# Kernel tuning notes

Hardware: AMD Instinct MI355X
Metric: run time of the kernel (lower is better)

## Reference

```python
import jax, jax.numpy as jnp
import numpy as np

ALPHA = 0.2  # leakyrelu negative slope

def setup_inputs() -> dict:
    key = jax.random.key(0)
    k1, k2, k3 = jax.random.split(key, 3)
    N, F_in, F_out = 8192, 512, 256
    input_x = jax.random.normal(k1, (N, F_in), dtype=jnp.float32)
    # xavier-ish scaling for params
    W = jax.random.normal(k2, (F_in, F_out), dtype=jnp.float32) * (1.414 * (2.0 / (F_in + F_out)) ** 0.5)
    a = jax.random.normal(k3, (2 * F_out, 1), dtype=jnp.float32) * (1.414 * (2.0 / (2 * F_out + 1)) ** 0.5)
    return {"input_x": input_x, "W": W, "a": a}

def reference(input_x, W, a):
    # h: [N, F_out]
    h = input_x @ W
    F_out = W.shape[1]
    # e_ij = leakyrelu([h_i || h_j] @ a) = leakyrelu(h_i @ a1 + h_j @ a2)
    s1 = h @ a[:F_out, 0]   # [N] contribution of row node i
    s2 = h @ a[F_out:, 0]   # [N] contribution of col node j
    e = jax.nn.leaky_relu(s1[:, None] + s2[None, :], negative_slope=ALPHA)  # [N, N]
    attention = jax.nn.softmax(e, axis=1)
    # dropout p=0.0 (eval) -> identity
    h_prime = attention @ h  # [N, F_out]
    return jax.nn.elu(h_prime)  # concat=True
```

## Files before the change

### kernel.cpp

```cpp
#include <hip/hip_runtime.h>
#include <hip/hip_bf16.h>

#define N_NODES 8192
#define F_IN    512
#define F_OUT   256
#define ALPHA   0.2f
#define CHUNK   32
#define NCHUNK  (N_NODES / CHUNK)
#define SEG     1024
#define BM      128
#define BN      64
#define BK      16

__global__ __launch_bounds__(512) void gemm_h(const float* __restrict__ A,
                                              const float* __restrict__ B,
                                              float* __restrict__ C) {
    __shared__ float As[BK][BM + 4];
    __shared__ float Bs[BK][BN + 4];
    const int t  = threadIdx.x;
    const int m0 = blockIdx.y * BM;
    const int n0 = blockIdx.x * BN;

    const int ar = t >> 2;
    const int ak = (t & 3) * 4;
    const int br = t >> 4;
    const int bc = (t & 15) * 4;

    const int ty = t >> 4;
    const int tx = t & 15;

    float4 aReg = *(const float4*)(A + (size_t)(m0 + ar) * F_IN + ak);
    float4 bReg = make_float4(0.f, 0.f, 0.f, 0.f);
    if (t < 256) bReg = *(const float4*)(B + (size_t)br * F_OUT + n0 + bc);

    float acc[4][4] = {};

    for (int k0 = 0; k0 < F_IN; k0 += BK) {
        __syncthreads();
        As[ak + 0][ar] = aReg.x;
        As[ak + 1][ar] = aReg.y;
        As[ak + 2][ar] = aReg.z;
        As[ak + 3][ar] = aReg.w;
        if (t < 256) *(float4*)(&Bs[br][bc]) = bReg;
        __syncthreads();
        if (k0 + BK < F_IN) {
            aReg = *(const float4*)(A + (size_t)(m0 + ar) * F_IN + k0 + BK + ak);
            if (t < 256) bReg = *(const float4*)(B + (size_t)(k0 + BK + br) * F_OUT + n0 + bc);
        }
        #pragma unroll
        for (int k = 0; k < BK; ++k) {
            const float4 a4 = *(const float4*)(&As[k][ty * 4]);
            const float4 b4 = *(const float4*)(&Bs[k][tx * 4]);
            acc[0][0] += a4.x * b4.x; acc[0][1] += a4.x * b4.y;
            acc[0][2] += a4.x * b4.z; acc[0][3] += a4.x * b4.w;
            acc[1][0] += a4.y * b4.x; acc[1][1] += a4.y * b4.y;
            acc[1][2] += a4.y * b4.z; acc[1][3] += a4.y * b4.w;
            acc[2][0] += a4.z * b4.x; acc[2][1] += a4.z * b4.y;
            acc[2][2] += a4.z * b4.z; acc[2][3] += a4.z * b4.w;
            acc[3][0] += a4.w * b4.x; acc[3][1] += a4.w * b4.y;
            acc[3][2] += a4.w * b4.z; acc[3][3] += a4.w * b4.w;
        }
    }
    #pragma unroll
    for (int r = 0; r < 4; ++r) {
        float4 o = make_float4(acc[r][0], acc[r][1], acc[r][2], acc[r][3]);
        *(float4*)(C + (size_t)(m0 + ty * 4 + r) * F_OUT + n0 + tx * 4) = o;
    }
}

__global__ __launch_bounds__(256) void s12_kernel(const float* __restrict__ h,
                                                  const float* __restrict__ a,
                                                  float* __restrict__ s1,
                                                  float* __restrict__ s2) {
    const int wave = threadIdx.x >> 6;
    const int lane = threadIdx.x & 63;
    const int row  = blockIdx.x * 4 + wave;

    const float4 hv = *(const float4*)(h + (size_t)row * F_OUT + lane * 4);
    const float4 a1 = *(const float4*)(a + lane * 4);
    const float4 a2 = *(const float4*)(a + F_OUT + lane * 4);

    float p1 = hv.x * a1.x + hv.y * a1.y + hv.z * a1.z + hv.w * a1.w;
    float p2 = hv.x * a2.x + hv.y * a2.y + hv.z * a2.z + hv.w * a2.w;
    #pragma unroll
    for (int off = 32; off; off >>= 1) {
        p1 += __shfl_xor(p1, off);
        p2 += __shfl_xor(p2, off);
    }
    if (lane == 0) { s1[row] = p1; s2[row] = p2; }
}

__global__ __launch_bounds__(1024) void seg_sort(const float* __restrict__ s2,
                                                 float* __restrict__ v,
                                                 int* __restrict__ p) {
    __shared__ float sv[SEG];
    __shared__ int   sp[SEG];
    const int t    = threadIdx.x;
    const int base = blockIdx.x * SEG;
    sv[t] = s2[base + t];
    sp[t] = base + t;
    __syncthreads();
    for (int k = 2; k <= SEG; k <<= 1) {
        for (int j = k >> 1; j > 0; j >>= 1) {
            const int ixj = t ^ j;
            if (ixj > t) {
                const bool up = ((t & k) == 0);
                const float av = sv[t], bv = sv[ixj];
                if (up ? (av > bv) : (av < bv)) {
                    sv[t] = bv; sv[ixj] = av;
                    const int pa = sp[t]; sp[t] = sp[ixj]; sp[ixj] = pa;
                }
            }
            __syncthreads();
        }
    }
    v[base + t] = sv[t];
    p[base + t] = sp[t];
}

__global__ __launch_bounds__(256) void merge_pass(const float* __restrict__ vin,
                                                  const int* __restrict__ pin,
                                                  float* __restrict__ vout,
                                                  int* __restrict__ pout,
                                                  int L) {
    const int gid   = blockIdx.x * 256 + threadIdx.x;
    const int pair  = gid / (2 * L);
    const int local = gid - pair * 2 * L;
    const int beg   = pair * 2 * L;

    if (local < L) {
        const int i     = local;
        const float key = vin[beg + i];
        const int  idx  = pin[beg + i];
        const float* Brun = vin + beg + L;
        int lo = 0, hi = L;
        while (lo < hi) {
            const int mid = (lo + hi) >> 1;
            if (Brun[mid] < key) lo = mid + 1; else hi = mid;
        }
        vout[beg + i + lo] = key;
        pout[beg + i + lo] = idx;
    } else {
        const int i     = local - L;
        const float key = vin[beg + L + i];
        const int  idx  = pin[beg + L + i];
        const float* Arun = vin + beg;
        int lo = 0, hi = L;
        while (lo < hi) {
            const int mid = (lo + hi) >> 1;
            if (Arun[mid] <= key) lo = mid + 1; else hi = mid;
        }
        vout[beg + lo + i] = key;
        pout[beg + lo + i] = idx;
    }
}

__global__ __launch_bounds__(256) void chunk_sums(const float* __restrict__ h,
                                                  const float* __restrict__ v,
                                                  const int* __restrict__ p,
                                                  float* __restrict__ cneg,
                                                  float* __restrict__ cpos,
                                                  float* __restrict__ czn,
                                                  float* __restrict__ czp) {
    const int c = blockIdx.x;
    const int f = threadIdx.x;
    const float M = v[N_NODES - 1];
    float accN = 0.f, accP = 0.f, zn = 0.f, zp = 0.f;
    #pragma unroll 8
    for (int tt = 0; tt < CHUNK; ++tt) {
        const int j = c * CHUNK + tt;
        const float vj = v[j];
        const int pj   = p[j];
        const float wn = __expf(ALPHA * vj);
        const float wp = __expf(vj - M);
        const float hv = h[(size_t)pj * F_OUT + f];
        accN += wn * hv; accP += wp * hv;
        zn += wn; zp += wp;
    }
    cneg[c * F_OUT + f] = accN;
    cpos[c * F_OUT + f] = accP;
    if (f == 0) { czn[c] = zn; czp[c] = zp; }
}

__global__ __launch_bounds__(256) void scan_cols(float* __restrict__ cneg,
                                                 float* __restrict__ cpos,
                                                 float* __restrict__ czn,
                                                 float* __restrict__ czp) {
    const int f = blockIdx.x;
    const int c = threadIdx.x;
    __shared__ float bn[NCHUNK];
    __shared__ float bp[NCHUNK];

    const float xn = cneg[(size_t)c * F_OUT + f];
    const float xp = cpos[(size_t)c * F_OUT + f];
    bn[c] = xn; bp[c] = xp;
    __syncthreads();
    #pragma unroll
    for (int off = 1; off < NCHUNK; off <<= 1) {
        const float an = (c >= off) ? bn[c - off] : 0.f;
        const float ap = (c + off < NCHUNK) ? bp[c + off] : 0.f;
        __syncthreads();
        bn[c] += an; bp[c] += ap;
        __syncthreads();
    }
    cneg[(size_t)c * F_OUT + f] = bn[c] - xn;
    cpos[(size_t)c * F_OUT + f] = bp[c] - xp;

    if (blockIdx.x == 0) {
        __shared__ float sn[NCHUNK];
        __shared__ float sp_[NCHUNK];
        const float yn = czn[c];
        const float yp = czp[c];
        sn[c] = yn; sp_[c] = yp;
        __syncthreads();
        #pragma unroll
        for (int off = 1; off < NCHUNK; off <<= 1) {
            const float an = (c >= off) ? sn[c - off] : 0.f;
            const float ap = (c + off < NCHUNK) ? sp_[c + off] : 0.f;
            __syncthreads();
            sn[c] += an; sp_[c] += ap;
            __syncthreads();
        }
        czn[c] = sn[c] - yn;
        czp[c] = sp_[c] - yp;
    }
}

__global__ __launch_bounds__(256) void rows2_kernel(const float* __restrict__ s1,
                                                    const float* __restrict__ v,
                                                    const int* __restrict__ p,
                                                    const float* __restrict__ h,
                                                    const float* __restrict__ cnegS,
                                                    const float* __restrict__ cposS,
                                                    const float* __restrict__ cznS,
                                                    const float* __restrict__ czpS,
                                                    float* __restrict__ out) {
    const int wave = threadIdx.x >> 6;
    const int lane = threadIdx.x & 63;
    const int i = blockIdx.x * 4 + wave;

    const float s1v = s1[i];
    const float M   = v[N_NODES - 1];

    const float thr = -s1v;
    int lo = 0, hi = N_NODES;
    while (lo < hi) {
        const int mid = (lo + hi) >> 1;
        if (v[mid] < thr) lo = mid + 1; else hi = mid;
    }
    const int k = lo;
    const int c = min(k >> 5, NCHUNK - 1);
    const int start = c * CHUNK;

    const float4 bN = *(const float4*)(cnegS + (size_t)c * F_OUT + lane * 4);
    const float4 bP = *(const float4*)(cposS + (size_t)c * F_OUT + lane * 4);
    float aN0 = bN.x, aN1 = bN.y, aN2 = bN.z, aN3 = bN.w;
    float aP0 = bP.x, aP1 = bP.y, aP2 = bP.z, aP3 = bP.w;
    float zn = cznS[c];
    float zp = czpS[c];

    #pragma unroll 8
    for (int tt = 0; tt < CHUNK; ++tt) {
        const int j = start + tt;
        const float vj = v[j];
        const int pj   = p[j];
        const float4 hv = *(const float4*)(h + (size_t)pj * F_OUT + lane * 4);
        if (j < k) {
            const float wn = __expf(ALPHA * vj);
            aN0 += wn * hv.x; aN1 += wn * hv.y; aN2 += wn * hv.z; aN3 += wn * hv.w;
            zn += wn;
        } else {
            const float wp = __expf(vj - M);
            aP0 += wp * hv.x; aP1 += wp * hv.y; aP2 += wp * hv.z; aP3 += wp * hv.w;
            zp += wp;
        }
    }

    const float x  = s1v + M;
    const float m  = (x >= 0.f) ? x : ALPHA * x;
    const float cp = __expf(x - m);
    const float cn = __expf(ALPHA * s1v - m);

    const float invZ = 1.0f / (cp * zp + cn * zn);

    float4 o;
    o.x = (cp * aP0 + cn * aN0) * invZ;
    o.y = (cp * aP1 + cn * aN1) * invZ;
    o.z = (cp * aP2 + cn * aN2) * invZ;
    o.w = (cp * aP3 + cn * aN3) * invZ;
    o.x = (o.x > 0.f) ? o.x : expm1f(o.x);
    o.y = (o.y > 0.f) ? o.y : expm1f(o.y);
    o.z = (o.z > 0.f) ? o.z : expm1f(o.z);
    o.w = (o.w > 0.f) ? o.w : expm1f(o.w);
    *(float4*)(out + (size_t)i * F_OUT + lane * 4) = o;
}

__global__ __launch_bounds__(1024) void maxs2_kernel(const float* __restrict__ s2,
                                                     float* __restrict__ M) {
    __shared__ float red[1024];
    float m = -1e30f;
    for (int i = threadIdx.x; i < N_NODES; i += 1024) m = fmaxf(m, s2[i]);
    red[threadIdx.x] = m;
    __syncthreads();
    for (int s = 512; s; s >>= 1) {
        if (threadIdx.x < s) red[threadIdx.x] = fmaxf(red[threadIdx.x], red[threadIdx.x + s]);
        __syncthreads();
    }
    if (threadIdx.x == 0) M[0] = red[0];
}

__global__ __launch_bounds__(256) void aggregate_kernel(const float* __restrict__ h,
                                                        const float* __restrict__ s1,
                                                        const float* __restrict__ s2,
                                                        const float* __restrict__ Mptr,
                                                        float* __restrict__ out) {
    __shared__ float w_lds[32][33];
    __shared__ float s2t[32];
    __shared__ float s1_loc[32];
    __shared__ float m_loc[32];

    const int t  = threadIdx.x;
    const int i0 = blockIdx.x * 32;
    const float Mv = Mptr[0];

    if (t < 32) {
        const float s1v = s1[i0 + t];
        s1_loc[t] = s1v;
        const float x = s1v + Mv;
        m_loc[t] = (x >= 0.f) ? x : ALPHA * x;
    }
    __syncthreads();

    const int g  = t >> 6;
    const int fl = t & 63;
    const int f4 = fl * 4;

    float acc[8][4] = {};
    float zacc[8]   = {};

    for (int j0 = 0; j0 < N_NODES; j0 += 32) {
        __syncthreads();
        if (t < 32) s2t[t] = s2[j0 + t];
        __syncthreads();
        #pragma unroll
        for (int q = 0; q < 4; ++q) {
            const int idx = t + q * 256;
            const int il  = idx >> 5;
            const int jl  = idx & 31;
            float e = s1_loc[il] + s2t[jl];
            e = (e >= 0.f) ? e : ALPHA * e;
            w_lds[il][jl] = __expf(e - m_loc[il]);
        }
        __syncthreads();

        #pragma unroll 4
        for (int jl = 0; jl < 32; ++jl) {
            const float4 hv = *(const float4*)(h + (size_t)(j0 + jl) * F_OUT + f4);
            #pragma unroll
            for (int r = 0; r < 8; ++r) {
                const float w = w_lds[g * 8 + r][jl];
                acc[r][0] += w * hv.x;
                acc[r][1] += w * hv.y;
                acc[r][2] += w * hv.z;
                acc[r][3] += w * hv.w;
                zacc[r]   += w;
            }
        }
    }

    #pragma unroll
    for (int r = 0; r < 8; ++r) {
        const int i = i0 + g * 8 + r;
        const float inv = 1.0f / zacc[r];
        float4 o;
        o.x = acc[r][0] * inv; o.y = acc[r][1] * inv;
        o.z = acc[r][2] * inv; o.w = acc[r][3] * inv;
        o.x = (o.x > 0.f) ? o.x : expm1f(o.x);
        o.y = (o.y > 0.f) ? o.y : expm1f(o.y);
        o.z = (o.z > 0.f) ? o.z : expm1f(o.z);
        o.w = (o.w > 0.f) ? o.w : expm1f(o.w);
        *(float4*)(out + (size_t)i * F_OUT + f4) = o;
    }
}

extern "C" void kernel_launch(void* const* d_in, const int* in_sizes, int n_in,
                              void* d_out, int out_size, void* d_ws, size_t ws_size,
                              hipStream_t stream) {
    const float* x = (const float*)d_in[0];
    const float* W = (const float*)d_in[1];
    const float* a = (const float*)d_in[2];
    float* out = (float*)d_out;

    constexpr size_t SZ_H    = (size_t)N_NODES * F_OUT * 4;
    constexpr size_t SZ_VEC  = (size_t)N_NODES * 4;
    constexpr size_t SZ_CHNK = (size_t)NCHUNK * F_OUT * 4;
    constexpr size_t SZ_CZ   = (size_t)NCHUNK * 4;

    constexpr size_t OFF_H     = 0;
    constexpr size_t OFF_S1    = OFF_H + SZ_H;
    constexpr size_t OFF_S2    = OFF_S1 + SZ_VEC;
    constexpr size_t OFF_V0    = OFF_S2 + SZ_VEC;
    constexpr size_t OFF_P0    = OFF_V0 + SZ_VEC;
    constexpr size_t OFF_V1    = OFF_P0 + SZ_VEC;
    constexpr size_t OFF_P1    = OFF_V1 + SZ_VEC;
    constexpr size_t OFF_CZN   = OFF_P1 + SZ_VEC;
    constexpr size_t OFF_CZP   = OFF_CZN + SZ_CZ;
    constexpr size_t OFF_CNEG  = OFF_CZP + SZ_CZ;
    constexpr size_t OFF_CPOS  = OFF_CNEG + SZ_CHNK;
    constexpr size_t REQUIRED  = OFF_CPOS + SZ_CHNK;

    char* ws = (char*)d_ws;
    float* h  = (float*)(ws + OFF_H);
    float* s1 = (float*)(ws + OFF_S1);
    float* s2 = (float*)(ws + OFF_S2);

    gemm_h<<<dim3(F_OUT / BN, N_NODES / BM), 512, 0, stream>>>(x, W, h);
    s12_kernel<<<N_NODES / 4, 256, 0, stream>>>(h, a, s1, s2);

    if (ws_size >= REQUIRED) {
        float* v0    = (float*)(ws + OFF_V0);
        int*   p0    = (int*)(ws + OFF_P0);
        float* v1    = (float*)(ws + OFF_V1);
        int*   p1    = (int*)(ws + OFF_P1);
        float* czn   = (float*)(ws + OFF_CZN);
        float* czp   = (float*)(ws + OFF_CZP);
        float* cneg  = (float*)(ws + OFF_CNEG);
        float* cpos  = (float*)(ws + OFF_CPOS);

        seg_sort<<<N_NODES / SEG, SEG, 0, stream>>>(s2, v0, p0);
        merge_pass<<<N_NODES / 256, 256, 0, stream>>>(v0, p0, v1, p1, 1024);
        merge_pass<<<N_NODES / 256, 256, 0, stream>>>(v1, p1, v0, p0, 2048);
        merge_pass<<<N_NODES / 256, 256, 0, stream>>>(v0, p0, v1, p1, 4096);

        chunk_sums<<<NCHUNK, 256, 0, stream>>>(h, v1, p1, cneg, cpos, czn, czp);
        scan_cols<<<F_OUT, NCHUNK, 0, stream>>>(cneg, cpos, czn, czp);
        rows2_kernel<<<N_NODES / 4, 256, 0, stream>>>(s1, v1, p1, h,
                                                      cneg, cpos, czn, czp, out);
    } else {
        float* M = (float*)(ws + OFF_V0);
        maxs2_kernel<<<1, 1024, 0, stream>>>(s2, M);
        aggregate_kernel<<<N_NODES / 32, 256, 0, stream>>>(h, s1, s2, M, out);
    }
}
```

Baseline: 164.0 us.

## Fuse post-GEMM stages into one cooperative kernel with grid syncs

Replaces the s12, segmented sort, three merge passes, chunk sums, column scan and row aggregation launches with a single cooperative mega-kernel of 256 blocks that separates the stages with grid-wide syncs. The intent is to remove per-launch overhead and inter-kernel gaps across about eight small dependent kernels. In exchange, the bitonic sort now runs on only 8 blocks of 256 threads, each handling 4 elements per thread. Aggregation uses 256 blocks looping over 8 rows per wave, so the heavy phases get less parallelism than the original 2048-block launches.

```diff
diff --git a/kernel.cpp b/kernel.cpp
--- a/kernel.cpp
+++ b/kernel.cpp
@@ -1,5 +1,8 @@
 #include <hip/hip_runtime.h>
 #include <hip/hip_bf16.h>
+#include <hip/hip_cooperative_groups.h>
+
+namespace cg = cooperative_groups;
 
 #define N_NODES 8192
 #define F_IN    512
@@ -25,7 +28,6 @@
     const int ak = (t & 3) * 4;
     const int br = t >> 4;
     const int bc = (t & 15) * 4;
-
     const int ty = t >> 4;
     const int tx = t & 15;
 
@@ -68,6 +70,230 @@
     }
 }
 
+__global__ __launch_bounds__(256) void mega_kernel(
+        const float* __restrict__ h,
+        const float* __restrict__ a,
+        float* __restrict__ s1, float* __restrict__ s2,
+        float* __restrict__ v0, int* __restrict__ p0,
+        float* __restrict__ v1, int* __restrict__ p1,
+        float* __restrict__ cneg, float* __restrict__ cpos,
+        float* __restrict__ czn,  float* __restrict__ czp,
+        float* __restrict__ out) {
+    cg::grid_group grid = cg::this_grid();
+    const int t    = threadIdx.x;
+    const int bid  = blockIdx.x;
+    const int wave = t >> 6;
+    const int lane = t & 63;
+
+    __shared__ float sv[SEG];
+    __shared__ int   sp[SEG];
+    __shared__ float bn[NCHUNK];
+    __shared__ float bp[NCHUNK];
+    __shared__ float sn[NCHUNK];
+    __shared__ float sz[NCHUNK];
+
+    {
+        const float4 a1 = *(const float4*)(a + lane * 4);
+        const float4 a2 = *(const float4*)(a + F_OUT + lane * 4);
+        #pragma unroll
+        for (int r = 0; r < 8; ++r) {
+            const int row = bid * 32 + wave * 8 + r;
+            const float4 hv = *(const float4*)(h + (size_t)row * F_OUT + lane * 4);
+            float d1 = hv.x * a1.x + hv.y * a1.y + hv.z * a1.z + hv.w * a1.w;
+            float d2 = hv.x * a2.x + hv.y * a2.y + hv.z * a2.z + hv.w * a2.w;
+            #pragma unroll
+            for (int off = 32; off; off >>= 1) {
+                d1 += __shfl_xor(d1, off);
+                d2 += __shfl_xor(d2, off);
+            }
+            if (lane == 0) { s1[row] = d1; s2[row] = d2; }
+        }
+    }
+    grid.sync();
+
+    if (bid < N_NODES / SEG) {
+        const int base = bid * SEG;
+        for (int i = t; i < SEG; i += 256) { sv[i] = s2[base + i]; sp[i] = base + i; }
+        __syncthreads();
+        for (int k = 2; k <= SEG; k <<= 1) {
+            for (int j = k >> 1; j > 0; j >>= 1) {
+                for (int i = t; i < SEG; i += 256) {
+                    const int ixj = i ^ j;
+                    if (ixj > i) {
+                        const bool up = ((i & k) == 0);
+                        const float av = sv[i], bv = sv[ixj];
+                        if (up ? (av > bv) : (av < bv)) {
+                            sv[i] = bv; sv[ixj] = av;
+                            const int pa = sp[i]; sp[i] = sp[ixj]; sp[ixj] = pa;
+                        }
+                    }
+                }
+                __syncthreads();
+            }
+        }
+        for (int i = t; i < SEG; i += 256) { v0[base + i] = sv[i]; p0[base + i] = sp[i]; }
+    }
+    grid.sync();
+
+    {
+        const int gid = bid * 256 + t;
+        const float* vin; const int* pin; float* vout; int* pout;
+        #pragma unroll 1
+        for (int pass = 0; pass < 3; ++pass) {
+            const int L = SEG << pass;
+            if (pass == 0) { vin = v0; pin = p0; vout = v1; pout = p1; }
+            else if (pass == 1) { vin = v1; pin = p1; vout = v0; pout = p0; }
+            else { vin = v0; pin = p0; vout = v1; pout = p1; }
+            if (gid < N_NODES) {
+                const int pair  = gid / (2 * L);
+                const int local = gid - pair * 2 * L;
+                const int beg   = pair * 2 * L;
+                if (local < L) {
+                    const int i     = local;
+                    const float key = vin[beg + i];
+                    const int  idx  = pin[beg + i];
+                    const float* Brun = vin + beg + L;
+                    int lo = 0, hi = L;
+                    while (lo < hi) {
+                        const int mid = (lo + hi) >> 1;
+                        if (Brun[mid] < key) lo = mid + 1; else hi = mid;
+                    }
+                    vout[beg + i + lo] = key;
+                    pout[beg + i + lo] = idx;
+                } else {
+                    const int i     = local - L;
+                    const float key = vin[beg + L + i];
+                    const int  idx  = pin[beg + L + i];
+                    const float* Arun = vin + beg;
+                    int lo = 0, hi = L;
+                    while (lo < hi) {
+                        const int mid = (lo + hi) >> 1;
+                        if (Arun[mid] <= key) lo = mid + 1; else hi = mid;
+                    }
+                    vout[beg + lo + i] = key;
+                    pout[beg + lo + i] = idx;
+                }
+            }
+            grid.sync();
+        }
+    }
+
+    {
+        const float M = v1[N_NODES - 1];
+        float accN = 0.f, accP = 0.f, zn = 0.f, zp = 0.f;
+        #pragma unroll 8
+        for (int tt = 0; tt < CHUNK; ++tt) {
+            const int j = bid * CHUNK + tt;
+            const float vj = v1[j];
+            const int pj   = p1[j];
+            const float wn = __expf(ALPHA * vj);
+            const float wp = __expf(vj - M);
+            const float hv = h[(size_t)pj * F_OUT + t];
+            accN += wn * hv; accP += wp * hv;
+            zn += wn; zp += wp;
+        }
+        cneg[bid * F_OUT + t] = accN;
+        cpos[bid * F_OUT + t] = accP;
+        if (t == 0) { czn[bid] = zn; czp[bid] = zp; }
+    }
+    grid.sync();
+
+    {
+        const float xn = cneg[(size_t)t * F_OUT + bid];
+        const float xp = cpos[(size_t)t * F_OUT + bid];
+        bn[t] = xn; bp[t] = xp;
+        __syncthreads();
+        #pragma unroll
+        for (int off = 1; off < NCHUNK; off <<= 1) {
+            const float an = (t >= off) ? bn[t - off] : 0.f;
+            const float ap = (t + off < NCHUNK) ? bp[t + off] : 0.f;
+            __syncthreads();
+            bn[t] += an; bp[t] += ap;
+            __syncthreads();
+        }
+        cneg[(size_t)t * F_OUT + bid] = bn[t] - xn;
+        cpos[(size_t)t * F_OUT + bid] = bp[t] - xp;
+
+        if (bid == 0) {
+            const float yn = czn[t];
+            const float yp = czp[t];
+            sn[t] = yn; sz[t] = yp;
+            __syncthreads();
+            #pragma unroll
+            for (int off = 1; off < NCHUNK; off <<= 1) {
+                const float an = (t >= off) ? sn[t - off] : 0.f;
+                const float ap = (t + off < NCHUNK) ? sz[t + off] : 0.f;
+                __syncthreads();
+                sn[t] += an; sz[t] += ap;
+                __syncthreads();
+            }
+            czn[t] = sn[t] - yn;
+            czp[t] = sz[t] - yp;
+        }
+    }
+    grid.sync();
+
+    {
+        const float M = v1[N_NODES - 1];
+        #pragma unroll 1
+        for (int r = 0; r < 8; ++r) {
+            const int i = bid * 32 + wave * 8 + r;
+            const float s1v = s1[i];
+
+            const float thr = -s1v;
+            int lo = 0, hi = N_NODES;
+            while (lo < hi) {
+                const int mid = (lo + hi) >> 1;
+                if (v1[mid] < thr) lo = mid + 1; else hi = mid;
+            }
+            const int k = lo;
+            const int c = min(k >> 5, NCHUNK - 1);
+            const int start = c * CHUNK;
+
+            const float4 bN = *(const float4*)(cneg + (size_t)c * F_OUT + lane * 4);
+            const float4 bP = *(const float4*)(cpos + (size_t)c * F_OUT + lane * 4);
+            float aN0 = bN.x, aN1 = bN.y, aN2 = bN.z, aN3 = bN.w;
+            float aP0 = bP.x, aP1 = bP.y, aP2 = bP.z, aP3 = bP.w;
+            float zn = czn[c];
+            float zp = czp[c];
+
+            #pragma unroll 8
+            for (int tt = 0; tt < CHUNK; ++tt) {
+                const int j = start + tt;
+                const float vj = v1[j];
+                const int pj   = p1[j];
+                const float4 hv = *(const float4*)(h + (size_t)pj * F_OUT + lane * 4);
+                if (j < k) {
+                    const float wn = __expf(ALPHA * vj);
+                    aN0 += wn * hv.x; aN1 += wn * hv.y; aN2 += wn * hv.z; aN3 += wn * hv.w;
+                    zn += wn;
+                } else {
+                    const float wp = __expf(vj - M);
+                    aP0 += wp * hv.x; aP1 += wp * hv.y; aP2 += wp * hv.z; aP3 += wp * hv.w;
+                    zp += wp;
+                }
+            }
+
+            const float x  = s1v + M;
+            const float m  = (x >= 0.f) ? x : ALPHA * x;
+            const float cp = __expf(x - m);
+            const float cn = __expf(ALPHA * s1v - m);
+            const float invZ = 1.0f / (cp * zp + cn * zn);
+
+            float4 o;
+            o.x = (cp * aP0 + cn * aN0) * invZ;
+            o.y = (cp * aP1 + cn * aN1) * invZ;
+            o.z = (cp * aP2 + cn * aN2) * invZ;
+            o.w = (cp * aP3 + cn * aN3) * invZ;
+            o.x = (o.x > 0.f) ? o.x : expm1f(o.x);
+            o.y = (o.y > 0.f) ? o.y : expm1f(o.y);
+            o.z = (o.z > 0.f) ? o.z : expm1f(o.z);
+            o.w = (o.w > 0.f) ? o.w : expm1f(o.w);
+            *(float4*)(out + (size_t)i * F_OUT + lane * 4) = o;
+        }
+    }
+}
+
 __global__ __launch_bounds__(256) void s12_kernel(const float* __restrict__ h,
                                                   const float* __restrict__ a,
                                                   float* __restrict__ s1,
@@ -88,211 +314,6 @@
         p2 += __shfl_xor(p2, off);
     }
     if (lane == 0) { s1[row] = p1; s2[row] = p2; }
-}
-
-__global__ __launch_bounds__(1024) void seg_sort(const float* __restrict__ s2,
-                                                 float* __restrict__ v,
-                                                 int* __restrict__ p) {
-    __shared__ float sv[SEG];
-    __shared__ int   sp[SEG];
-    const int t    = threadIdx.x;
-    const int base = blockIdx.x * SEG;
-    sv[t] = s2[base + t];
-    sp[t] = base + t;
-    __syncthreads();
-    for (int k = 2; k <= SEG; k <<= 1) {
-        for (int j = k >> 1; j > 0; j >>= 1) {
-            const int ixj = t ^ j;
-            if (ixj > t) {
-                const bool up = ((t & k) == 0);
-                const float av = sv[t], bv = sv[ixj];
-                if (up ? (av > bv) : (av < bv)) {
-                    sv[t] = bv; sv[ixj] = av;
-                    const int pa = sp[t]; sp[t] = sp[ixj]; sp[ixj] = pa;
-                }
-            }
-            __syncthreads();
-        }
-    }
-    v[base + t] = sv[t];
-    p[base + t] = sp[t];
-}
-
-__global__ __launch_bounds__(256) void merge_pass(const float* __restrict__ vin,
-                                                  const int* __restrict__ pin,
-                                                  float* __restrict__ vout,
-                                                  int* __restrict__ pout,
-                                                  int L) {
-    const int gid   = blockIdx.x * 256 + threadIdx.x;
-    const int pair  = gid / (2 * L);
-    const int local = gid - pair * 2 * L;
-    const int beg   = pair * 2 * L;
-
-    if (local < L) {
-        const int i     = local;
-        const float key = vin[beg + i];
-        const int  idx  = pin[beg + i];
-        const float* Brun = vin + beg + L;
-        int lo = 0, hi = L;
-        while (lo < hi) {
-            const int mid = (lo + hi) >> 1;
-            if (Brun[mid] < key) lo = mid + 1; else hi = mid;
-        }
-        vout[beg + i + lo] = key;
-        pout[beg + i + lo] = idx;
-    } else {
-        const int i     = local - L;
-        const float key = vin[beg + L + i];
-        const int  idx  = pin[beg + L + i];
-        const float* Arun = vin + beg;
-        int lo = 0, hi = L;
-        while (lo < hi) {
-            const int mid = (lo + hi) >> 1;
-            if (Arun[mid] <= key) lo = mid + 1; else hi = mid;
-        }
-        vout[beg + lo + i] = key;
-        pout[beg + lo + i] = idx;
-    }
-}
-
-__global__ __launch_bounds__(256) void chunk_sums(const float* __restrict__ h,
-                                                  const float* __restrict__ v,
-                                                  const int* __restrict__ p,
-                                                  float* __restrict__ cneg,
-                                                  float* __restrict__ cpos,
-                                                  float* __restrict__ czn,
-                                                  float* __restrict__ czp) {
-    const int c = blockIdx.x;
-    const int f = threadIdx.x;
-    const float M = v[N_NODES - 1];
-    float accN = 0.f, accP = 0.f, zn = 0.f, zp = 0.f;
-    #pragma unroll 8
-    for (int tt = 0; tt < CHUNK; ++tt) {
-        const int j = c * CHUNK + tt;
-        const float vj = v[j];
-        const int pj   = p[j];
-        const float wn = __expf(ALPHA * vj);
-        const float wp = __expf(vj - M);
-        const float hv = h[(size_t)pj * F_OUT + f];
-        accN += wn * hv; accP += wp * hv;
-        zn += wn; zp += wp;
-    }
-    cneg[c * F_OUT + f] = accN;
-    cpos[c * F_OUT + f] = accP;
-    if (f == 0) { czn[c] = zn; czp[c] = zp; }
-}
-
-__global__ __launch_bounds__(256) void scan_cols(float* __restrict__ cneg,
-                                                 float* __restrict__ cpos,
-                                                 float* __restrict__ czn,
-                                                 float* __restrict__ czp) {
-    const int f = blockIdx.x;
-    const int c = threadIdx.x;
-    __shared__ float bn[NCHUNK];
-    __shared__ float bp[NCHUNK];
-
-    const float xn = cneg[(size_t)c * F_OUT + f];
-    const float xp = cpos[(size_t)c * F_OUT + f];
-    bn[c] = xn; bp[c] = xp;
-    __syncthreads();
-    #pragma unroll
-    for (int off = 1; off < NCHUNK; off <<= 1) {
-        const float an = (c >= off) ? bn[c - off] : 0.f;
-        const float ap = (c + off < NCHUNK) ? bp[c + off] : 0.f;
-        __syncthreads();
-        bn[c] += an; bp[c] += ap;
-        __syncthreads();
-    }
-    cneg[(size_t)c * F_OUT + f] = bn[c] - xn;
-    cpos[(size_t)c * F_OUT + f] = bp[c] - xp;
-
-    if (blockIdx.x == 0) {
-        __shared__ float sn[NCHUNK];
-        __shared__ float sp_[NCHUNK];
-        const float yn = czn[c];
-        const float yp = czp[c];
-        sn[c] = yn; sp_[c] = yp;
-        __syncthreads();
-        #pragma unroll
-        for (int off = 1; off < NCHUNK; off <<= 1) {
-            const float an = (c >= off) ? sn[c - off] : 0.f;
-            const float ap = (c + off < NCHUNK) ? sp_[c + off] : 0.f;
-            __syncthreads();
-            sn[c] += an; sp_[c] += ap;
-            __syncthreads();
-        }
-        czn[c] = sn[c] - yn;
-        czp[c] = sp_[c] - yp;
-    }
-}
-
-__global__ __launch_bounds__(256) void rows2_kernel(const float* __restrict__ s1,
-                                                    const float* __restrict__ v,
-                                                    const int* __restrict__ p,
-                                                    const float* __restrict__ h,
-                                                    const float* __restrict__ cnegS,
-                                                    const float* __restrict__ cposS,
-                                                    const float* __restrict__ cznS,
-                                                    const float* __restrict__ czpS,
-                                                    float* __restrict__ out) {
-    const int wave = threadIdx.x >> 6;
-    const int lane = threadIdx.x & 63;
-    const int i = blockIdx.x * 4 + wave;
-
-    const float s1v = s1[i];
-    const float M   = v[N_NODES - 1];
-
-    const float thr = -s1v;
-    int lo = 0, hi = N_NODES;
-    while (lo < hi) {
-        const int mid = (lo + hi) >> 1;
-        if (v[mid] < thr) lo = mid + 1; else hi = mid;
-    }
-    const int k = lo;
-    const int c = min(k >> 5, NCHUNK - 1);
-    const int start = c * CHUNK;
-
-    const float4 bN = *(const float4*)(cnegS + (size_t)c * F_OUT + lane * 4);
-    const float4 bP = *(const float4*)(cposS + (size_t)c * F_OUT + lane * 4);
-    float aN0 = bN.x, aN1 = bN.y, aN2 = bN.z, aN3 = bN.w;
-    float aP0 = bP.x, aP1 = bP.y, aP2 = bP.z, aP3 = bP.w;
-    float zn = cznS[c];
-    float zp = czpS[c];
-
-    #pragma unroll 8
-    for (int tt = 0; tt < CHUNK; ++tt) {
-        const int j = start + tt;
-        const float vj = v[j];
-        const int pj   = p[j];
-        const float4 hv = *(const float4*)(h + (size_t)pj * F_OUT + lane * 4);
-        if (j < k) {
-            const float wn = __expf(ALPHA * vj);
-            aN0 += wn * hv.x; aN1 += wn * hv.y; aN2 += wn * hv.z; aN3 += wn * hv.w;
-            zn += wn;
-        } else {
-            const float wp = __expf(vj - M);
-            aP0 += wp * hv.x; aP1 += wp * hv.y; aP2 += wp * hv.z; aP3 += wp * hv.w;
-            zp += wp;
-        }
-    }
-
-    const float x  = s1v + M;
-    const float m  = (x >= 0.f) ? x : ALPHA * x;
-    const float cp = __expf(x - m);
-    const float cn = __expf(ALPHA * s1v - m);
-
-    const float invZ = 1.0f / (cp * zp + cn * zn);
-
-    float4 o;
-    o.x = (cp * aP0 + cn * aN0) * invZ;
-    o.y = (cp * aP1 + cn * aN1) * invZ;
-    o.z = (cp * aP2 + cn * aN2) * invZ;
-    o.w = (cp * aP3 + cn * aN3) * invZ;
-    o.x = (o.x > 0.f) ? o.x : expm1f(o.x);
-    o.y = (o.y > 0.f) ? o.y : expm1f(o.y);
-    o.z = (o.z > 0.f) ? o.z : expm1f(o.z);
-    o.w = (o.w > 0.f) ? o.w : expm1f(o.w);
-    *(float4*)(out + (size_t)i * F_OUT + lane * 4) = o;
 }
 
 __global__ __launch_bounds__(1024) void maxs2_kernel(const float* __restrict__ s2,
@@ -415,7 +436,6 @@
     float* s2 = (float*)(ws + OFF_S2);
 
     gemm_h<<<dim3(F_OUT / BN, N_NODES / BM), 512, 0, stream>>>(x, W, h);
-    s12_kernel<<<N_NODES / 4, 256, 0, stream>>>(h, a, s1, s2);
 
     if (ws_size >= REQUIRED) {
         float* v0    = (float*)(ws + OFF_V0);
@@ -427,17 +447,15 @@
         float* cneg  = (float*)(ws + OFF_CNEG);
         float* cpos  = (float*)(ws + OFF_CPOS);
 
-        seg_sort<<<N_NODES / SEG, SEG, 0, stream>>>(s2, v0, p0);
-        merge_pass<<<N_NODES / 256, 256, 0, stream>>>(v0, p0, v1, p1, 1024);
-        merge_pass<<<N_NODES / 256, 256, 0, stream>>>(v1, p1, v0, p0, 2048);
-        merge_pass<<<N_NODES / 256, 256, 0, stream>>>(v0, p0, v1, p1, 4096);
-
-        chunk_sums<<<NCHUNK, 256, 0, stream>>>(h, v1, p1, cneg, cpos, czn, czp);
-        scan_cols<<<F_OUT, NCHUNK, 0, stream>>>(cneg, cpos, czn, czp);
-        rows2_kernel<<<N_NODES / 4, 256, 0, stream>>>(s1, v1, p1, h,
-                                                      cneg, cpos, czn, czp, out);
+        void* args[] = { (void*)&h, (void*)&a, (void*)&s1, (void*)&s2,
+                         (void*)&v0, (void*)&p0, (void*)&v1, (void*)&p1,
+                         (void*)&cneg, (void*)&cpos, (void*)&czn, (void*)&czp,
+                         (void*)&out };
+        hipLaunchCooperativeKernel((void*)mega_kernel, dim3(256), dim3(256),
+                                   args, 0, stream);
     } else {
         float* M = (float*)(ws + OFF_V0);
+        s12_kernel<<<N_NODES / 4, 256, 0, stream>>>(h, a, s1, s2);
         maxs2_kernel<<<1, 1024, 0, stream>>>(s2, M);
         aggregate_kernel<<<N_NODES / 32, 256, 0, stream>>>(h, s1, s2, M, out);
     }
```

Result: slower. 489.9 us (+198.8%).

## Fuse s1/s2 projection into GEMM epilogue and pre-permute h for row pass

Applied to the files above, without the earlier changes.

Folds the attention-vector dot products into the GEMM epilogue: each thread reduces its 4x4 tile against a1/a2, does a 16-lane shuffle reduction, and atomically adds into s1/s2, which are zeroed by a memset first. This drops the separate s12 kernel and its reread of h. The chunk-sum kernel now also writes h in sorted order, so the row kernel reads contiguous rows instead of gathering through the permutation. The cost is float atomics (nondeterministic summation order), an extra memset launch, and an extra 8MB write of permuted h.

```diff
diff --git a/kernel.cpp b/kernel.cpp
--- a/kernel.cpp
+++ b/kernel.cpp
@@ -12,9 +12,12 @@
 #define BN      64
 #define BK      16
 
-__global__ __launch_bounds__(512) void gemm_h(const float* __restrict__ A,
-                                              const float* __restrict__ B,
-                                              float* __restrict__ C) {
+__global__ __launch_bounds__(512) void gemm_s12(const float* __restrict__ A,
+                                                const float* __restrict__ B,
+                                                const float* __restrict__ attn,
+                                                float* __restrict__ C,
+                                                float* __restrict__ s1,
+                                                float* __restrict__ s2) {
     __shared__ float As[BK][BM + 4];
     __shared__ float Bs[BK][BN + 4];
     const int t  = threadIdx.x;
@@ -25,7 +28,6 @@
     const int ak = (t & 3) * 4;
     const int br = t >> 4;
     const int bc = (t & 15) * 4;
-
     const int ty = t >> 4;
     const int tx = t & 15;
 
@@ -66,28 +68,25 @@
         float4 o = make_float4(acc[r][0], acc[r][1], acc[r][2], acc[r][3]);
         *(float4*)(C + (size_t)(m0 + ty * 4 + r) * F_OUT + n0 + tx * 4) = o;
     }
-}
-
-__global__ __launch_bounds__(256) void s12_kernel(const float* __restrict__ h,
-                                                  const float* __restrict__ a,
-                                                  float* __restrict__ s1,
-                                                  float* __restrict__ s2) {
-    const int wave = threadIdx.x >> 6;
-    const int lane = threadIdx.x & 63;
-    const int row  = blockIdx.x * 4 + wave;
-
-    const float4 hv = *(const float4*)(h + (size_t)row * F_OUT + lane * 4);
-    const float4 a1 = *(const float4*)(a + lane * 4);
-    const float4 a2 = *(const float4*)(a + F_OUT + lane * 4);
-
-    float p1 = hv.x * a1.x + hv.y * a1.y + hv.z * a1.z + hv.w * a1.w;
-    float p2 = hv.x * a2.x + hv.y * a2.y + hv.z * a2.z + hv.w * a2.w;
+
+    const float4 a1v = *(const float4*)(attn + n0 + tx * 4);
+    const float4 a2v = *(const float4*)(attn + F_OUT + n0 + tx * 4);
     #pragma unroll
-    for (int off = 32; off; off >>= 1) {
-        p1 += __shfl_xor(p1, off);
-        p2 += __shfl_xor(p2, off);
-    }
-    if (lane == 0) { s1[row] = p1; s2[row] = p2; }
+    for (int r = 0; r < 4; ++r) {
+        float p1 = acc[r][0] * a1v.x + acc[r][1] * a1v.y
+                 + acc[r][2] * a1v.z + acc[r][3] * a1v.w;
+        float p2 = acc[r][0] * a2v.x + acc[r][1] * a2v.y
+                 + acc[r][2] * a2v.z + acc[r][3] * a2v.w;
+        #pragma unroll
+        for (int off = 8; off; off >>= 1) {
+            p1 += __shfl_xor(p1, off);
+            p2 += __shfl_xor(p2, off);
+        }
+        if (tx == 0) {
+            atomicAdd(&s1[m0 + ty * 4 + r], p1);
+            atomicAdd(&s2[m0 + ty * 4 + r], p2);
+        }
+    }
 }
 
 __global__ __launch_bounds__(1024) void seg_sort(const float* __restrict__ s2,
@@ -155,13 +154,14 @@
     }
 }
 
-__global__ __launch_bounds__(256) void chunk_sums(const float* __restrict__ h,
-                                                  const float* __restrict__ v,
-                                                  const int* __restrict__ p,
-                                                  float* __restrict__ cneg,
-                                                  float* __restrict__ cpos,
-                                                  float* __restrict__ czn,
-                                                  float* __restrict__ czp) {
+__global__ __launch_bounds__(256) void chunk_perm_sums(const float* __restrict__ h,
+                                                       const float* __restrict__ v,
+                                                       const int* __restrict__ p,
+                                                       float* __restrict__ hs,
+                                                       float* __restrict__ cneg,
+                                                       float* __restrict__ cpos,
+                                                       float* __restrict__ czn,
+                                                       float* __restrict__ czp) {
     const int c = blockIdx.x;
     const int f = threadIdx.x;
     const float M = v[N_NODES - 1];
@@ -174,6 +174,7 @@
         const float wn = __expf(ALPHA * vj);
         const float wp = __expf(vj - M);
         const float hv = h[(size_t)pj * F_OUT + f];
+        hs[(size_t)j * F_OUT + f] = hv;
         accN += wn * hv; accP += wp * hv;
         zn += wn; zp += wp;
     }
@@ -226,10 +227,9 @@
     }
 }
 
-__global__ __launch_bounds__(256) void rows2_kernel(const float* __restrict__ s1,
+__global__ __launch_bounds__(256) void rows3_kernel(const float* __restrict__ s1,
                                                     const float* __restrict__ v,
-                                                    const int* __restrict__ p,
-                                                    const float* __restrict__ h,
+                                                    const float* __restrict__ hs,
                                                     const float* __restrict__ cnegS,
                                                     const float* __restrict__ cposS,
                                                     const float* __restrict__ cznS,
@@ -263,8 +263,7 @@
     for (int tt = 0; tt < CHUNK; ++tt) {
         const int j = start + tt;
         const float vj = v[j];
-        const int pj   = p[j];
-        const float4 hv = *(const float4*)(h + (size_t)pj * F_OUT + lane * 4);
+        const float4 hv = *(const float4*)(hs + (size_t)j * F_OUT + lane * 4);
         if (j < k) {
             const float wn = __expf(ALPHA * vj);
             aN0 += wn * hv.x; aN1 += wn * hv.y; aN2 += wn * hv.z; aN3 += wn * hv.w;
@@ -280,7 +279,6 @@
     const float m  = (x >= 0.f) ? x : ALPHA * x;
     const float cp = __expf(x - m);
     const float cn = __expf(ALPHA * s1v - m);
-
     const float invZ = 1.0f / (cp * zp + cn * zn);
 
     float4 o;
@@ -407,15 +405,17 @@
     constexpr size_t OFF_CZP   = OFF_CZN + SZ_CZ;
     constexpr size_t OFF_CNEG  = OFF_CZP + SZ_CZ;
     constexpr size_t OFF_CPOS  = OFF_CNEG + SZ_CHNK;
-    constexpr size_t REQUIRED  = OFF_CPOS + SZ_CHNK;
+    constexpr size_t OFF_HS    = OFF_CPOS + SZ_CHNK;
+    constexpr size_t REQUIRED  = OFF_HS + SZ_H;
 
     char* ws = (char*)d_ws;
     float* h  = (float*)(ws + OFF_H);
     float* s1 = (float*)(ws + OFF_S1);
     float* s2 = (float*)(ws + OFF_S2);
 
-    gemm_h<<<dim3(F_OUT / BN, N_NODES / BM), 512, 0, stream>>>(x, W, h);
-    s12_kernel<<<N_NODES / 4, 256, 0, stream>>>(h, a, s1, s2);
+    hipMemsetAsync(s1, 0, 2 * SZ_VEC, stream);
+
+    gemm_s12<<<dim3(F_OUT / BN, N_NODES / BM), 512, 0, stream>>>(x, W, a, h, s1, s2);
 
     if (ws_size >= REQUIRED) {
         float* v0    = (float*)(ws + OFF_V0);
@@ -426,15 +426,17 @@
         float* czp   = (float*)(ws + OFF_CZP);
         float* cneg  = (float*)(ws + OFF_CNEG);
         float* cpos  = (float*)(ws + OFF_CPOS);
+        float* hs    = (float*)(ws + OFF_HS);
 
         seg_sort<<<N_NODES / SEG, SEG, 0, stream>>>(s2, v0, p0);
         merge_pass<<<N_NODES / 256, 256, 0, stream>>>(v0, p0, v1, p1, 1024);
         merge_pass<<<N_NODES / 256, 256, 0, stream>>>(v1, p1, v0, p0, 2048);
         merge_pass<<<N_NODES / 256, 256, 0, stream>>>(v0, p0, v1, p1, 4096);
 
-        chunk_sums<<<NCHUNK, 256, 0, stream>>>(h, v1, p1, cneg, cpos, czn, czp);
+        chunk_perm_sums<<<NCHUNK, 256, 0, stream>>>(h, v1, p1, hs,
+                                                    cneg, cpos, czn, czp);
         scan_cols<<<F_OUT, NCHUNK, 0, stream>>>(cneg, cpos, czn, czp);
-        rows2_kernel<<<N_NODES / 4, 256, 0, stream>>>(s1, v1, p1, h,
+        rows3_kernel<<<N_NODES / 4, 256, 0, stream>>>(s1, v1, hs,
                                                       cneg, cpos, czn, czp, out);
     } else {
         float* M = (float*)(ws + OFF_V0);
```

After: 159.0 us. -3.1%, faster.
